# Kernel optimization log

Hardware: AMD Instinct MI355X
Metric: run time of the kernel (lower is better)

## Reference

```python
import jax, jax.numpy as jnp
import numpy as np

D_IN = 1024
D_OUT = 1024

def setup_inputs() -> dict:
    key = jax.random.key(0)
    ks = jax.random.split(key, 7)
    s = 1.0 / np.sqrt(D_IN)
    x = jax.random.normal(ks[0], (4, 2048, D_IN), dtype=jnp.float32)
    Wq = jax.random.uniform(ks[1], (D_IN, D_OUT), jnp.float32, -s, s)
    Wk = jax.random.uniform(ks[2], (D_IN, D_OUT), jnp.float32, -s, s)
    Wv = jax.random.uniform(ks[3], (D_IN, D_OUT), jnp.float32, -s, s)
    bq = jax.random.uniform(ks[4], (D_OUT,), jnp.float32, -s, s)
    bk = jax.random.uniform(ks[5], (D_OUT,), jnp.float32, -s, s)
    bv = jax.random.uniform(ks[6], (D_OUT,), jnp.float32, -s, s)
    return {"x": x, "Wq": Wq, "Wk": Wk, "Wv": Wv, "bq": bq, "bk": bk, "bv": bv}

def reference(x, Wq, Wk, Wv, bq, bk, bv):
    # x: [b, n, d_in]
    q = jnp.einsum('bnd,de->bne', x, Wq) + bq
    k = jnp.einsum('bnd,de->bne', x, Wk) + bk
    v = jnp.einsum('bnd,de->bne', x, Wv) + bv
    scale = 1.0 / jnp.sqrt(jnp.asarray(k.shape[-1], dtype=x.dtype))
    scores = jnp.einsum('bqe,bke->bqk', q, k) * scale  # [b, n, n]
    weights = jax.nn.softmax(scores, axis=-1)
    return jnp.einsum('bqk,bke->bqe', weights, v)
```

## Files before the change

kernel.cpp:

```cpp
#include <hip/hip_runtime.h>
#include <cstdint>

typedef __bf16 bf16x8 __attribute__((ext_vector_type(8)));
typedef float f32x16 __attribute__((ext_vector_type(16)));

__device__ __forceinline__ unsigned short f2b(float f) {
    union { float f; uint32_t u; } x; x.f = f;
    uint32_t r = (x.u + 0x7fffu + ((x.u >> 16) & 1u)) >> 16;
    return (unsigned short)r;
}
__device__ __forceinline__ float b2f(unsigned short h) {
    union { float f; uint32_t u; } x; x.u = ((uint32_t)h) << 16;
    return x.f;
}

__global__ __launch_bounds__(256) void convert_x_kernel(const float* __restrict__ x,
                                                        unsigned short* __restrict__ xb) {
    int i = (blockIdx.x * 256 + threadIdx.x) * 4;
    float4 v = *(const float4*)(x + i);
    ushort4 o;
    o.x = f2b(v.x); o.y = f2b(v.y); o.z = f2b(v.z); o.w = f2b(v.w);
    *(ushort4*)(xb + i) = o;
}

__global__ __launch_bounds__(1024) void transpose_w_kernel(const float* __restrict__ Wq,
                                                           const float* __restrict__ Wk,
                                                           const float* __restrict__ Wv,
                                                           unsigned short* __restrict__ Wt) {
    __shared__ float tile[32][33];
    const float* W = (blockIdx.z == 0) ? Wq : (blockIdx.z == 1) ? Wk : Wv;
    int n0 = blockIdx.x * 32, k0 = blockIdx.y * 32;
    int tx = threadIdx.x, ty = threadIdx.y;
    tile[ty][tx] = W[(k0 + ty) * 1024 + n0 + tx];
    __syncthreads();
    Wt[((long)blockIdx.z * 1024 + n0 + ty) * 1024 + k0 + tx] = f2b(tile[tx][ty]);
}

template <int EPI>
__global__ __launch_bounds__(256) void gemm32(const unsigned short* __restrict__ A, int lda, long sA,
                                              const unsigned short* __restrict__ Bm, int ldb, long sB,
                                              void* __restrict__ Cv, long sC, int K,
                                              const float* __restrict__ bq, const float* __restrict__ bk,
                                              const float* __restrict__ bv,
                                              unsigned short* __restrict__ Qb,
                                              unsigned short* __restrict__ Kb,
                                              unsigned short* __restrict__ Vt) {
    __shared__ unsigned short As[128 * 64];
    __shared__ unsigned short Bs[128 * 64];

    const int tid = threadIdx.x;
    const int wave = tid >> 6, lane = tid & 63;
    const int h = lane >> 5;
    const int l31 = lane & 31;
    const int wm = wave >> 1, wn = wave & 1;
    const long bm = (long)blockIdx.y * 128;
    const long bn = (long)blockIdx.x * 128;

    const unsigned short* Ab = A + (long)blockIdx.z * sA;
    const unsigned short* Bb = Bm + (long)blockIdx.z * sB;

    f32x16 acc[2][2];
#pragma unroll
    for (int mi = 0; mi < 2; ++mi)
#pragma unroll
        for (int ni = 0; ni < 2; ++ni)
#pragma unroll
            for (int r = 0; r < 16; ++r) acc[mi][ni][r] = 0.0f;

    const int srow_in = lane >> 3;
    const int cswz = (lane & 7) ^ srow_in;
    const unsigned short* aptr[4];
    const unsigned short* bptr[4];
    unsigned short* asl[4];
    unsigned short* bsl[4];
#pragma unroll
    for (int j = 0; j < 4; ++j) {
        const int row = j * 32 + wave * 8 + srow_in;
        aptr[j] = Ab + (bm + row) * (long)lda + cswz * 8;
        bptr[j] = Bb + (bn + row) * (long)ldb + cswz * 8;
        asl[j] = &As[(j * 32 + wave * 8) * 64];
        bsl[j] = &Bs[(j * 32 + wave * 8) * 64];
    }

    const int arow0 = (wm * 64 + l31) * 64;
    const int brow0 = (wn * 64 + l31) * 64;
    int sw[4];
#pragma unroll
    for (int kh = 0; kh < 4; ++kh)
        sw[kh] = (((2 * kh + h) ^ (lane & 7)) * 8);

    for (int k0 = 0; k0 < K; k0 += 64) {
#pragma unroll
        for (int j = 0; j < 4; ++j) {
            __builtin_amdgcn_global_load_lds((const __attribute__((address_space(1))) void*)(aptr[j] + k0),
                                             (__attribute__((address_space(3))) void*)asl[j], 16, 0, 0);
            __builtin_amdgcn_global_load_lds((const __attribute__((address_space(1))) void*)(bptr[j] + k0),
                                             (__attribute__((address_space(3))) void*)bsl[j], 16, 0, 0);
        }
        __syncthreads();

#pragma unroll
        for (int kp = 0; kp < 2; ++kp) {
            bf16x8 af[2][2], bfr[2][2];
#pragma unroll
            for (int mi = 0; mi < 2; ++mi)
#pragma unroll
                for (int kk = 0; kk < 2; ++kk)
                    af[mi][kk] = *(const bf16x8*)&As[arow0 + mi * 32 * 64 + sw[kp * 2 + kk]];
#pragma unroll
            for (int ni = 0; ni < 2; ++ni)
#pragma unroll
                for (int kk = 0; kk < 2; ++kk)
                    bfr[ni][kk] = *(const bf16x8*)&Bs[brow0 + ni * 32 * 64 + sw[kp * 2 + kk]];
#pragma unroll
            for (int kk = 0; kk < 2; ++kk)
#pragma unroll
                for (int mi = 0; mi < 2; ++mi)
#pragma unroll
                    for (int ni = 0; ni < 2; ++ni)
                        acc[mi][ni] = __builtin_amdgcn_mfma_f32_32x32x16_bf16(af[mi][kk], bfr[ni][kk],
                                                                              acc[mi][ni], 0, 0, 0);
        }
        __syncthreads();
    }

#pragma unroll
    for (int mi = 0; mi < 2; ++mi) {
#pragma unroll
        for (int ni = 0; ni < 2; ++ni) {
            const f32x16 a = acc[mi][ni];
            const long col = bn + wn * 64 + ni * 32 + l31;
            const long rowB = bm + wm * 64 + mi * 32 + h * 4;
            if constexpr (EPI == 0) {
                if (col < 1024) {
                    const float bias = bq[col];
#pragma unroll
                    for (int g = 0; g < 4; ++g)
#pragma unroll
                        for (int r = 0; r < 4; ++r)
                            Qb[(rowB + g * 8 + r) * 1024 + col] = f2b((a[g * 4 + r] + bias) * 0.03125f);
                } else if (col < 2048) {
                    const float bias = bk[col - 1024];
#pragma unroll
                    for (int g = 0; g < 4; ++g)
#pragma unroll
                        for (int r = 0; r < 4; ++r)
                            Kb[(rowB + g * 8 + r) * 1024 + (col - 1024)] = f2b(a[g * 4 + r] + bias);
                } else {
                    const float bias = bv[col - 2048];
#pragma unroll
                    for (int g = 0; g < 4; ++g) {
                        const long row0 = rowB + g * 8;
                        const long batch = row0 >> 11;
                        const int n = (int)(row0 & 2047);
                        ushort4 o;
                        o.x = f2b(a[g * 4 + 0] + bias);
                        o.y = f2b(a[g * 4 + 1] + bias);
                        o.z = f2b(a[g * 4 + 2] + bias);
                        o.w = f2b(a[g * 4 + 3] + bias);
                        *(ushort4*)&Vt[(batch * 1024 + (col - 2048)) * 2048 + n] = o;
                    }
                }
            } else if constexpr (EPI == 1) {
                unsigned short* S = (unsigned short*)Cv + (long)blockIdx.z * sC;
#pragma unroll
                for (int g = 0; g < 4; ++g)
#pragma unroll
                    for (int r = 0; r < 4; ++r)
                        S[(rowB + g * 8 + r) * 2048 + col] = f2b(a[g * 4 + r]);
            } else {
                float* O = (float*)Cv + (long)blockIdx.z * sC;
#pragma unroll
                for (int g = 0; g < 4; ++g)
#pragma unroll
                    for (int r = 0; r < 4; ++r)
                        O[(rowB + g * 8 + r) * 1024 + col] = a[g * 4 + r];
            }
        }
    }
}

__global__ __launch_bounds__(256) void softmax_kernel(unsigned short* __restrict__ S) {
    const long row = blockIdx.x;
    unsigned short* p = S + row * 2048;
    const int tid = threadIdx.x;
    const int wave = tid >> 6, lane = tid & 63;

    ushort4 u0 = *(const ushort4*)&p[tid * 8];
    ushort4 u1 = *(const ushort4*)&p[tid * 8 + 4];
    float v[8];
    v[0] = b2f(u0.x); v[1] = b2f(u0.y); v[2] = b2f(u0.z); v[3] = b2f(u0.w);
    v[4] = b2f(u1.x); v[5] = b2f(u1.y); v[6] = b2f(u1.z); v[7] = b2f(u1.w);

    float m = v[0];
#pragma unroll
    for (int j = 1; j < 8; ++j) m = fmaxf(m, v[j]);
#pragma unroll
    for (int off = 32; off; off >>= 1) m = fmaxf(m, __shfl_xor(m, off, 64));
    __shared__ float redm[4];
    __shared__ float reds[4];
    if (lane == 0) redm[wave] = m;
    __syncthreads();
    m = fmaxf(fmaxf(redm[0], redm[1]), fmaxf(redm[2], redm[3]));

    float s = 0.0f;
#pragma unroll
    for (int j = 0; j < 8; ++j) { v[j] = __expf(v[j] - m); s += v[j]; }
#pragma unroll
    for (int off = 32; off; off >>= 1) s += __shfl_xor(s, off, 64);
    if (lane == 0) reds[wave] = s;
    __syncthreads();
    s = reds[0] + reds[1] + reds[2] + reds[3];
    const float inv = 1.0f / s;

    u0.x = f2b(v[0] * inv); u0.y = f2b(v[1] * inv); u0.z = f2b(v[2] * inv); u0.w = f2b(v[3] * inv);
    u1.x = f2b(v[4] * inv); u1.y = f2b(v[5] * inv); u1.z = f2b(v[6] * inv); u1.w = f2b(v[7] * inv);
    *(ushort4*)&p[tid * 8] = u0;
    *(ushort4*)&p[tid * 8 + 4] = u1;
}

extern "C" void kernel_launch(void* const* d_in, const int* in_sizes, int n_in,
                              void* d_out, int out_size, void* d_ws, size_t ws_size,
                              hipStream_t stream) {
    const float* x  = (const float*)d_in[0];
    const float* Wq = (const float*)d_in[1];
    const float* Wk = (const float*)d_in[2];
    const float* Wv = (const float*)d_in[3];
    const float* bq = (const float*)d_in[4];
    const float* bk = (const float*)d_in[5];
    const float* bv = (const float*)d_in[6];
    float* out = (float*)d_out;

    char* ws = (char*)d_ws;
    unsigned short* xb = (unsigned short*)ws; ws += 8192L * 1024 * 2;
    unsigned short* Wt = (unsigned short*)ws; ws += 3072L * 1024 * 2;
    unsigned short* Qb = (unsigned short*)ws; ws += 8192L * 1024 * 2;
    unsigned short* Kb = (unsigned short*)ws; ws += 8192L * 1024 * 2;
    unsigned short* Vt = (unsigned short*)ws; ws += 4L * 1024 * 2048 * 2;
    unsigned short* S  = (unsigned short*)ws; ws += 4L * 2048 * 2048 * 2;

    convert_x_kernel<<<8192, 256, 0, stream>>>(x, xb);
    transpose_w_kernel<<<dim3(32, 32, 3), dim3(32, 32), 0, stream>>>(Wq, Wk, Wv, Wt);
    gemm32<0><<<dim3(24, 64, 1), 256, 0, stream>>>(xb, 1024, 0, Wt, 1024, 0,
                                                   nullptr, 0, 1024, bq, bk, bv, Qb, Kb, Vt);
    gemm32<1><<<dim3(16, 16, 4), 256, 0, stream>>>(Qb, 1024, 2048L * 1024, Kb, 1024, 2048L * 1024,
                                                   S, 2048L * 2048, 1024,
                                                   nullptr, nullptr, nullptr, nullptr, nullptr, nullptr);
    softmax_kernel<<<8192, 256, 0, stream>>>(S);
    gemm32<2><<<dim3(8, 16, 4), 256, 0, stream>>>(S, 2048, 2048L * 2048, Vt, 2048, 2048L * 1024,
                                                  out, 2048L * 1024, 2048,
                                                  nullptr, nullptr, nullptr, nullptr, nullptr, nullptr);
}
```

Before: 281.3 us.

## Double-buffer LDS tiles in bf16 GEMM to overlap global loads with MFMA

Splits shared memory into two ping-pong buffers for A and B and issues the next K-tile's global-to-LDS loads before computing on the current tile. The aim is to hide global load latency behind MFMA work instead of stalling at each barrier. This doubles LDS use to 64KB per block, which may reduce occupancy. The loop now steps K by 128 and assumes K is a multiple of 128.

```diff
diff --git a/kernel.cpp b/kernel.cpp
--- a/kernel.cpp
+++ b/kernel.cpp
@@ -45,8 +45,10 @@
                                               unsigned short* __restrict__ Qb,
                                               unsigned short* __restrict__ Kb,
                                               unsigned short* __restrict__ Vt) {
-    __shared__ unsigned short As[128 * 64];
-    __shared__ unsigned short Bs[128 * 64];
+    __shared__ unsigned short As0[128 * 64];
+    __shared__ unsigned short Bs0[128 * 64];
+    __shared__ unsigned short As1[128 * 64];
+    __shared__ unsigned short Bs1[128 * 64];
 
     const int tid = threadIdx.x;
     const int wave = tid >> 6, lane = tid & 63;
@@ -61,25 +63,25 @@
 
     f32x16 acc[2][2];
 #pragma unroll
-    for (int mi = 0; mi < 2; ++mi)
-#pragma unroll
-        for (int ni = 0; ni < 2; ++ni)
+    for (int mi = 0; mi < 2; ++mi) {
+#pragma unroll
+        for (int ni = 0; ni < 2; ++ni) {
 #pragma unroll
             for (int r = 0; r < 16; ++r) acc[mi][ni][r] = 0.0f;
+        }
+    }
 
     const int srow_in = lane >> 3;
     const int cswz = (lane & 7) ^ srow_in;
     const unsigned short* aptr[4];
     const unsigned short* bptr[4];
-    unsigned short* asl[4];
-    unsigned short* bsl[4];
+    int sloff[4];
 #pragma unroll
     for (int j = 0; j < 4; ++j) {
         const int row = j * 32 + wave * 8 + srow_in;
         aptr[j] = Ab + (bm + row) * (long)lda + cswz * 8;
         bptr[j] = Bb + (bn + row) * (long)ldb + cswz * 8;
-        asl[j] = &As[(j * 32 + wave * 8) * 64];
-        bsl[j] = &Bs[(j * 32 + wave * 8) * 64];
+        sloff[j] = (j * 32 + wave * 8) * 64;
     }
 
     const int arow0 = (wm * 64 + l31) * 64;
@@ -89,40 +91,65 @@
     for (int kh = 0; kh < 4; ++kh)
         sw[kh] = (((2 * kh + h) ^ (lane & 7)) * 8);
 
-    for (int k0 = 0; k0 < K; k0 += 64) {
-#pragma unroll
-        for (int j = 0; j < 4; ++j) {
-            __builtin_amdgcn_global_load_lds((const __attribute__((address_space(1))) void*)(aptr[j] + k0),
-                                             (__attribute__((address_space(3))) void*)asl[j], 16, 0, 0);
-            __builtin_amdgcn_global_load_lds((const __attribute__((address_space(1))) void*)(bptr[j] + k0),
-                                             (__attribute__((address_space(3))) void*)bsl[j], 16, 0, 0);
-        }
+#define STAGE(AsB, BsB, kofs)                                                                           \
+    do {                                                                                                \
+        _Pragma("unroll")                                                                               \
+        for (int j = 0; j < 4; ++j) {                                                                   \
+            __builtin_amdgcn_global_load_lds(                                                           \
+                (const __attribute__((address_space(1))) void*)(aptr[j] + (kofs)),                      \
+                (__attribute__((address_space(3))) void*)(&AsB[sloff[j]]), 16, 0, 0);                   \
+            __builtin_amdgcn_global_load_lds(                                                           \
+                (const __attribute__((address_space(1))) void*)(bptr[j] + (kofs)),                      \
+                (__attribute__((address_space(3))) void*)(&BsB[sloff[j]]), 16, 0, 0);                   \
+        }                                                                                               \
+    } while (0)
+
+#define COMPUTE_T(AsB, BsB)                                                                             \
+    do {                                                                                                \
+        _Pragma("unroll")                                                                               \
+        for (int kp = 0; kp < 2; ++kp) {                                                                \
+            bf16x8 af[2][2], bfr[2][2];                                                                 \
+            _Pragma("unroll")                                                                           \
+            for (int mi = 0; mi < 2; ++mi) {                                                            \
+                _Pragma("unroll")                                                                       \
+                for (int kk = 0; kk < 2; ++kk) {                                                        \
+                    af[mi][kk] = *(const bf16x8*)&AsB[arow0 + mi * 32 * 64 + sw[kp * 2 + kk]];          \
+                }                                                                                       \
+            }                                                                                           \
+            _Pragma("unroll")                                                                           \
+            for (int ni = 0; ni < 2; ++ni) {                                                            \
+                _Pragma("unroll")                                                                       \
+                for (int kk = 0; kk < 2; ++kk) {                                                        \
+                    bfr[ni][kk] = *(const bf16x8*)&BsB[brow0 + ni * 32 * 64 + sw[kp * 2 + kk]];         \
+                }                                                                                       \
+            }                                                                                           \
+            _Pragma("unroll")                                                                           \
+            for (int kk = 0; kk < 2; ++kk) {                                                            \
+                _Pragma("unroll")                                                                       \
+                for (int mi = 0; mi < 2; ++mi) {                                                        \
+                    _Pragma("unroll")                                                                   \
+                    for (int ni = 0; ni < 2; ++ni) {                                                    \
+                        acc[mi][ni] = __builtin_amdgcn_mfma_f32_32x32x16_bf16(af[mi][kk], bfr[ni][kk],  \
+                                                                              acc[mi][ni], 0, 0, 0);    \
+                    }                                                                                   \
+                }                                                                                       \
+            }                                                                                           \
+        }                                                                                               \
+    } while (0)
+
+    STAGE(As0, Bs0, 0);
+
+    for (int k0 = 0; k0 < K; k0 += 128) {
         __syncthreads();
-
-#pragma unroll
-        for (int kp = 0; kp < 2; ++kp) {
-            bf16x8 af[2][2], bfr[2][2];
-#pragma unroll
-            for (int mi = 0; mi < 2; ++mi)
-#pragma unroll
-                for (int kk = 0; kk < 2; ++kk)
-                    af[mi][kk] = *(const bf16x8*)&As[arow0 + mi * 32 * 64 + sw[kp * 2 + kk]];
-#pragma unroll
-            for (int ni = 0; ni < 2; ++ni)
-#pragma unroll
-                for (int kk = 0; kk < 2; ++kk)
-                    bfr[ni][kk] = *(const bf16x8*)&Bs[brow0 + ni * 32 * 64 + sw[kp * 2 + kk]];
-#pragma unroll
-            for (int kk = 0; kk < 2; ++kk)
-#pragma unroll
-                for (int mi = 0; mi < 2; ++mi)
-#pragma unroll
-                    for (int ni = 0; ni < 2; ++ni)
-                        acc[mi][ni] = __builtin_amdgcn_mfma_f32_32x32x16_bf16(af[mi][kk], bfr[ni][kk],
-                                                                              acc[mi][ni], 0, 0, 0);
-        }
+        STAGE(As1, Bs1, k0 + 64);
+        COMPUTE_T(As0, Bs0);
         __syncthreads();
-    }
+        if (k0 + 128 < K) STAGE(As0, Bs0, k0 + 128);
+        COMPUTE_T(As1, Bs1);
+    }
+
+#undef STAGE
+#undef COMPUTE_T
 
 #pragma unroll
     for (int mi = 0; mi < 2; ++mi) {
@@ -135,17 +162,19 @@
                 if (col < 1024) {
                     const float bias = bq[col];
 #pragma unroll
-                    for (int g = 0; g < 4; ++g)
+                    for (int g = 0; g < 4; ++g) {
 #pragma unroll
                         for (int r = 0; r < 4; ++r)
                             Qb[(rowB + g * 8 + r) * 1024 + col] = f2b((a[g * 4 + r] + bias) * 0.03125f);
+                    }
                 } else if (col < 2048) {
                     const float bias = bk[col - 1024];
 #pragma unroll
-                    for (int g = 0; g < 4; ++g)
+                    for (int g = 0; g < 4; ++g) {
 #pragma unroll
                         for (int r = 0; r < 4; ++r)
                             Kb[(rowB + g * 8 + r) * 1024 + (col - 1024)] = f2b(a[g * 4 + r] + bias);
+                    }
                 } else {
                     const float bias = bv[col - 2048];
 #pragma unroll
@@ -164,17 +193,19 @@
             } else if constexpr (EPI == 1) {
                 unsigned short* S = (unsigned short*)Cv + (long)blockIdx.z * sC;
 #pragma unroll
-                for (int g = 0; g < 4; ++g)
+                for (int g = 0; g < 4; ++g) {
 #pragma unroll
                     for (int r = 0; r < 4; ++r)
                         S[(rowB + g * 8 + r) * 2048 + col] = f2b(a[g * 4 + r]);
+                }
             } else {
                 float* O = (float*)Cv + (long)blockIdx.z * sC;
 #pragma unroll
-                for (int g = 0; g < 4; ++g)
+                for (int g = 0; g < 4; ++g) {
 #pragma unroll
                     for (int r = 0; r < 4; ++r)
                         O[(rowB + g * 8 + r) * 1024 + col] = a[g * 4 + r];
+                }
             }
         }
     }
```

After: 261.5 us. -7.0%, faster.
